# Optimization experiments

Measured on AMD Instinct MI355X. Metric: run time of the kernel, lower is better.

The kernel has to match this reference:

```python
import jax, jax.numpy as jnp
import numpy as np

B, NQ, NK = 16, 512, 1024
CQ, CV = 128, 128
H, D = 8, 64            # nb_heads, attention_size
SCALE = float(np.sqrt(D))


def setup_inputs() -> dict:
    key = jax.random.key(0)
    ks = jax.random.split(key, 10)
    s = 0.02
    return {
        "query": jax.random.normal(ks[0], (B, NQ, CQ), jnp.float32),
        "key": jax.random.normal(ks[1], (B, NK, CV), jnp.float32),
        "c_mask": jax.random.randint(ks[2], (B, NK), 0, 2).astype(jnp.float32),
        # torch Linear params, stored as [in, out] so y = x @ W + b
        "Wq": jax.random.normal(ks[3], (CQ, H * D), jnp.float32) * s,
        "bq": jnp.zeros((H * D,), jnp.float32),
        "Wk": jax.random.normal(ks[4], (CV, H * D), jnp.float32) * s,
        "bk": jnp.zeros((H * D,), jnp.float32),
        "Wv": jax.random.normal(ks[5], (CV, H * D), jnp.float32) * s,
        "bv": jnp.zeros((H * D,), jnp.float32),
    }


def reference(query, key, c_mask, Wq, bq, Wk, bk, Wv, bv):
    # projections -> [B, N, H, D]
    q = (query @ Wq + bq).reshape(B, NQ, H, D)
    k = (key @ Wk + bk).reshape(B, NK, H, D)
    v = (key @ Wv + bv).reshape(B, NK, H, D)
    # scaled scores [B, H, NQ, NK]
    scores = jnp.einsum('bqhd,bkhd->bhqk', q / SCALE, k)
    # additive mask: c_mask [B, NK] broadcasts over heads and queries
    scores = scores - 100000.0 * (1.0 - c_mask[:, None, None, :])
    attn = jax.nn.softmax(scores, axis=-1)
    # weighted values -> [B, NQ, H, D] -> concat heads
    c = jnp.einsum('bhqk,bkhd->bqhd', attn, v)
    return c.reshape(B, NQ, H * D)
```

## Files before the change

kernel.cpp:

```cpp
#include <hip/hip_runtime.h>
#include <hip/hip_bf16.h>

#define B_  16
#define NQ_ 512
#define NK_ 1024
#define CQ_ 128
#define H_  8
#define D_  64
#define HD_ 512

typedef __attribute__((ext_vector_type(8))) short short8;
typedef __attribute__((ext_vector_type(4))) float floatx4;

__device__ __forceinline__ short f2bf(float f) {
    union { float f; unsigned u; } x; x.f = f;
    unsigned r = (x.u + 0x7fffu + ((x.u >> 16) & 1u)) >> 16;
    return (short)r;
}
__device__ __forceinline__ int f2bf_pk(float a, float b) {
    __hip_bfloat162 h = __float22bfloat162_rn(make_float2(a, b));
    int r; __builtin_memcpy(&r, &h, 4); return r;
}
__device__ __forceinline__ short8 pack8(float4 a, float4 b) {
    union { int4 i; short8 s; } u;
    u.i = make_int4(f2bf_pk(a.x, a.y), f2bf_pk(a.z, a.w),
                    f2bf_pk(b.x, b.y), f2bf_pk(b.z, b.w));
    return u.s;
}
__device__ __forceinline__ int2 packi2(floatx4 a) {
    return make_int2(f2bf_pk(a[0], a[1]), f2bf_pk(a[2], a[3]));
}
__device__ __forceinline__ void async16(const short* g, short* l) {
    __builtin_amdgcn_global_load_lds(
        (const __attribute__((address_space(1))) void*)g,
        (__attribute__((address_space(3))) void*)l, 16, 0, 0);
}

__global__ __launch_bounds__(256) void prep_kernel(
    const float* __restrict__ W0, const float* __restrict__ W1,
    const float* __restrict__ W2, short* __restrict__ T0,
    short* __restrict__ T1, short* __restrict__ T2,
    const float* __restrict__ bq, float* __restrict__ bqs, float qscale)
{
    const int blk = blockIdx.x, t = threadIdx.x;
    if (blk == 48) {
        bqs[t]       = bq[t] * qscale;
        bqs[t + 256] = bq[t + 256] * qscale;
        return;
    }
    __shared__ short tsh[32 * 132];
    const int mat = blk >> 4, nb = blk & 15;
    const float* W = mat == 0 ? W0 : (mat == 1 ? W1 : W2);
    short* T = mat == 0 ? T0 : (mat == 1 ? T1 : T2);
    const float s = mat == 0 ? qscale : 1.0f;

    #pragma unroll
    for (int i = 0; i < 4; ++i) {
        const int idx = i * 256 + t;
        const int k = idx >> 3, c = (idx & 7) * 4;
        float4 v = *(const float4*)(W + (size_t)k * HD_ + nb * 32 + c);
        tsh[(c + 0) * 132 + k] = f2bf(v.x * s);
        tsh[(c + 1) * 132 + k] = f2bf(v.y * s);
        tsh[(c + 2) * 132 + k] = f2bf(v.z * s);
        tsh[(c + 3) * 132 + k] = f2bf(v.w * s);
    }
    __syncthreads();
    #pragma unroll
    for (int j = 0; j < 2; ++j) {
        const int idx = j * 256 + t;
        const int n = idx >> 4, seg = (idx & 15) * 8;
        *(short8*)(T + (size_t)(nb * 32 + n) * CQ_ + seg) =
            *(const short8*)&tsh[n * 132 + seg];
    }
}

__global__ __launch_bounds__(256, 2) void kvproj_kernel(
    const float* __restrict__ key_,
    const short* __restrict__ wkt, const short* __restrict__ wvt,
    const float* __restrict__ bk, const float* __restrict__ bv,
    short* __restrict__ ks, short* __restrict__ vt)
{
    __shared__ __align__(16) short csh[9216];

    int bx = blockIdx.x;
    const short* Wt; const float* bias; short* out; int transposed;
    if (bx < 128) { Wt = wkt; bias = bk; out = ks; transposed = 0; }
    else { bx -= 128; Wt = wvt; bias = bv; out = vt; transposed = 1; }

    const int tid  = threadIdx.x;
    const int w    = tid >> 6, lane = tid & 63;
    const int l15  = lane & 15, quad = lane >> 4;
    const int mbase = bx * 128;

    short8 afr[2][4];
    #pragma unroll
    for (int mt = 0; mt < 2; ++mt) {
        const float* xrow = key_ + (size_t)(mbase + w * 32 + mt * 16 + l15) * CQ_;
        #pragma unroll
        for (int kt = 0; kt < 4; ++kt)
            afr[mt][kt] = pack8(*(const float4*)(xrow + kt * 32 + quad * 8),
                                *(const float4*)(xrow + kt * 32 + quad * 8 + 4));
    }

    const int b  = mbase >> 10;
    const int r0 = mbase & 1023;

    #pragma unroll
    for (int hh = 0; hh < 4; ++hh) {
        const int h = blockIdx.y * 4 + hh;
        short8 bfr[4][4];
        #pragma unroll
        for (int nt = 0; nt < 4; ++nt) {
            const short8* wrow = (const short8*)(Wt + (size_t)(h * 64 + nt * 16 + l15) * CQ_);
            #pragma unroll
            for (int kt = 0; kt < 4; ++kt) bfr[nt][kt] = wrow[kt * 4 + quad];
        }
        floatx4 acc[2][4];
        #pragma unroll
        for (int mt = 0; mt < 2; ++mt)
            #pragma unroll
            for (int nt = 0; nt < 4; ++nt) {
                floatx4 a = {0.f, 0.f, 0.f, 0.f};
                #pragma unroll
                for (int kt = 0; kt < 4; ++kt)
                    a = __builtin_amdgcn_mfma_f32_16x16x32_bf16(afr[mt][kt], bfr[nt][kt], a, 0, 0, 0);
                acc[mt][nt] = a;
            }
        __syncthreads();
        #pragma unroll
        for (int mt = 0; mt < 2; ++mt)
            #pragma unroll
            for (int nt = 0; nt < 4; ++nt) {
                const float bvv = bias[h * 64 + nt * 16 + l15];
                #pragma unroll
                for (int i = 0; i < 4; ++i) {
                    const short s = f2bf(acc[mt][nt][i] + bvv);
                    const int m = w * 32 + mt * 16 + quad * 4 + i;
                    const int n = nt * 16 + l15;
                    if (!transposed) csh[m * 72 + n]  = s;
                    else             csh[n * 136 + m] = s;
                }
            }
        __syncthreads();

        const size_t bh = (size_t)(b * H_ + h);
        if (!transposed) {
            short* dst = out + (bh * NK_ + r0) * D_;
            #pragma unroll
            for (int it = 0; it < 4; ++it) {
                const int idx = it * 256 + tid;
                const int row = idx >> 3, c8 = (idx & 7) * 8;
                *(short8*)(dst + idx * 8) = *(const short8*)&csh[row * 72 + c8];
            }
        } else {
            short* dst = out + bh * D_ * NK_ + r0;
            #pragma unroll
            for (int it = 0; it < 4; ++it) {
                const int idx = it * 256 + tid;
                const int row = idx >> 4, c8 = (idx & 15) * 8;
                *(short8*)(dst + (size_t)row * NK_ + c8) = *(const short8*)&csh[row * 136 + c8];
            }
        }
    }
}

__global__ __launch_bounds__(256, 2) void attn_kernel(
    const float* __restrict__ query, const short* __restrict__ ks,
    const short* __restrict__ vt, const float* __restrict__ cmask,
    const short* __restrict__ wqt, const float* __restrict__ bqs,
    float* __restrict__ out)
{
    __shared__ __align__(16) short kbuf[2][2][64 * 64];
    __shared__ __align__(16) short vbuf[2][2][64 * 64];
    __shared__ __align__(16) short psh[128 * 64];

    const int tid = threadIdx.x;
    const int w = tid >> 6, lane = tid & 63;
    const int l15 = lane & 15, quad = lane >> 4;

    const int bx   = blockIdx.x;
    const int bh_i = bx & 127;
    const int qq   = bx >> 7;
    const int h    = bh_i & 7;
    const int b    = bh_i >> 3;

    const size_t bh = (size_t)bh_i;
    const short* kb_ = ks + bh * NK_ * D_;
    const short* vb  = vt + bh * D_ * NK_;
    const float* mk  = cmask + (size_t)b * NK_;

    short8 qa[2][2];
    {
        short8 waf[4][4];
        #pragma unroll
        for (int dt = 0; dt < 4; ++dt)
            #pragma unroll
            for (int kt = 0; kt < 4; ++kt)
                waf[dt][kt] = *(const short8*)(wqt + (size_t)(h * 64 + dt * 16 + l15) * CQ_ + kt * 32 + quad * 8);
        const int qr0 = qq * 128 + w * 32;
        #pragma unroll
        for (int g = 0; g < 2; ++g) {
            const float* qrow = query + ((size_t)b * NQ_ + qr0 + g * 16 + l15) * CQ_;
            short8 bqf[4];
            #pragma unroll
            for (int kt = 0; kt < 4; ++kt)
                bqf[kt] = pack8(*(const float4*)(qrow + kt * 32 + quad * 8),
                                *(const float4*)(qrow + kt * 32 + quad * 8 + 4));
            const int prow = w * 32 + g * 16 + l15;
            #pragma unroll
            for (int dt = 0; dt < 4; ++dt) {
                float4 bi = *(const float4*)(bqs + h * 64 + dt * 16 + quad * 4);
                floatx4 a = {bi.x, bi.y, bi.z, bi.w};
                #pragma unroll
                for (int kt = 0; kt < 4; ++kt)
                    a = __builtin_amdgcn_mfma_f32_16x16x32_bf16(waf[dt][kt], bqf[kt], a, 0, 0, 0);
                const int c16 = (dt * 2 + (quad >> 1)) ^ (prow & 7);
                *(int2*)&psh[prow * 64 + c16 * 8 + (quad & 1) * 4] = packi2(a);
            }
            qa[g][0] = *(const short8*)&psh[prow * 64 + ((quad    ) ^ (prow & 7)) * 8];
            qa[g][1] = *(const short8*)&psh[prow * 64 + ((4 + quad) ^ (prow & 7)) * 8];
        }
    }

    const int srow8 = lane >> 3, sc = lane & 7;
    auto stage = [&](int kb0, short (*kdst)[4096], short (*vdst)[4096]) {
        #pragma unroll
        for (int sub = 0; sub < 2; ++sub)
            #pragma unroll
            for (int j = 0; j < 2; ++j) {
                const int row = w * 16 + j * 8 + srow8;
                const int cs = sc ^ (row & 7);
                async16(kb_ + (size_t)(kb0 + sub * 64 + row) * D_ + cs * 8,
                        &kdst[sub][(w * 16 + j * 8) * 64]);
                async16(vb + (size_t)row * NK_ + kb0 + sub * 64 + cs * 8,
                        &vdst[sub][(w * 16 + j * 8) * 64]);
            }
    };

    float l_lane[2] = {0.f, 0.f};
    floatx4 o_acc[2][4];
    #pragma unroll
    for (int g = 0; g < 2; ++g)
        #pragma unroll
        for (int dt = 0; dt < 4; ++dt) o_acc[g][dt] = (floatx4){0.f, 0.f, 0.f, 0.f};

    stage(0, kbuf[0], vbuf[0]);
    __syncthreads();

    for (int ph = 0; ph < 8; ++ph) {
        const int cur = ph & 1;
        if (ph < 7) stage((ph + 1) * 128, kbuf[cur ^ 1], vbuf[cur ^ 1]);

        #pragma unroll
        for (int sub = 0; sub < 2; ++sub) {
            const short* kb  = kbuf[cur][sub];
            const short* vbl = vbuf[cur][sub];
            const int kbase = ph * 128 + sub * 64;

            short8 ka[4][2];
            #pragma unroll
            for (int nt = 0; nt < 4; ++nt) {
                const int row = nt * 16 + l15;
                ka[nt][0] = *(const short8*)&kb[row * 64 + ((quad    ) ^ (row & 7)) * 8];
                ka[nt][1] = *(const short8*)&kb[row * 64 + ((4 + quad) ^ (row & 7)) * 8];
            }
            short8 vf[2][4];
            #pragma unroll
            for (int dt = 0; dt < 4; ++dt) {
                const int row = dt * 16 + l15;
                vf[0][dt] = *(const short8*)&vbl[row * 64 + ((quad    ) ^ (row & 7)) * 8];
                vf[1][dt] = *(const short8*)&vbl[row * 64 + ((4 + quad) ^ (row & 7)) * 8];
            }
            float4 m4[4];
            #pragma unroll
            for (int nt = 0; nt < 4; ++nt)
                m4[nt] = *(const float4*)(mk + kbase + nt * 16 + quad * 4);

            #pragma unroll
            for (int g = 0; g < 2; ++g) {
                floatx4 st[4];
                #pragma unroll
                for (int nt = 0; nt < 4; ++nt) {
                    floatx4 a = {0.f, 0.f, 0.f, 0.f};
                    a = __builtin_amdgcn_mfma_f32_16x16x32_bf16(ka[nt][1], qa[g][1], a, 0, 0, 0);
                    a = __builtin_amdgcn_mfma_f32_16x16x32_bf16(ka[nt][0], qa[g][0], a, 0, 0, 0);
                    st[nt] = a;
                }
                const int prow = w * 32 + g * 16 + l15;
                float psum = 0.f;
                #pragma unroll
                for (int nt = 0; nt < 4; ++nt) {
                    float p0 = m4[nt].x * __builtin_amdgcn_exp2f(st[nt][0]);
                    float p1 = m4[nt].y * __builtin_amdgcn_exp2f(st[nt][1]);
                    float p2 = m4[nt].z * __builtin_amdgcn_exp2f(st[nt][2]);
                    float p3 = m4[nt].w * __builtin_amdgcn_exp2f(st[nt][3]);
                    psum += (p0 + p1) + (p2 + p3);
                    int2 pk = make_int2(f2bf_pk(p0, p1), f2bf_pk(p2, p3));
                    const int c16 = (2 * nt + (quad >> 1)) ^ (prow & 7);
                    *(int2*)&psh[prow * 64 + c16 * 8 + (quad & 1) * 4] = pk;
                }
                l_lane[g] += psum;
                #pragma unroll
                for (int kt = 0; kt < 2; ++kt) {
                    short8 pa = *(const short8*)&psh[prow * 64 + ((kt * 4 + quad) ^ (prow & 7)) * 8];
                    #pragma unroll
                    for (int dt = 0; dt < 4; ++dt)
                        o_acc[g][dt] = __builtin_amdgcn_mfma_f32_16x16x32_bf16(vf[kt][dt], pa, o_acc[g][dt], 0, 0, 0);
                }
            }
        }
        __syncthreads();
    }

    #pragma unroll
    for (int g = 0; g < 2; ++g) {
        float ls = l_lane[g];
        ls += __shfl_xor(ls, 16);
        ls += __shfl_xor(ls, 32);
        const float linv = 1.0f / ls;
        const int qr = qq * 128 + w * 32 + g * 16 + l15;
        float* orow = out + ((size_t)b * NQ_ + qr) * HD_ + h * D_;
        #pragma unroll
        for (int dt = 0; dt < 4; ++dt) {
            float4 v = make_float4(o_acc[g][dt][0] * linv, o_acc[g][dt][1] * linv,
                                   o_acc[g][dt][2] * linv, o_acc[g][dt][3] * linv);
            *(float4*)(orow + dt * 16 + quad * 4) = v;
        }
    }
}

extern "C" void kernel_launch(void* const* d_in, const int* in_sizes, int n_in,
                              void* d_out, int out_size, void* d_ws, size_t ws_size,
                              hipStream_t stream) {
    const float* query = (const float*)d_in[0];
    const float* key   = (const float*)d_in[1];
    const float* cmask = (const float*)d_in[2];
    const float* Wq    = (const float*)d_in[3];
    const float* bq    = (const float*)d_in[4];
    const float* Wk    = (const float*)d_in[5];
    const float* bk    = (const float*)d_in[6];
    const float* Wv    = (const float*)d_in[7];
    const float* bv    = (const float*)d_in[8];
    float* out = (float*)d_out;

    char* ws = (char*)d_ws;
    short* ks  = (short*)(ws);
    short* vt  = (short*)(ws + (size_t)(16u << 20));
    char*  w32 = ws + (size_t)(32u << 20);
    short* wqt = (short*)(w32);
    short* wkt = (short*)(w32 + 131072);
    short* wvt = (short*)(w32 + 131072 * 2);
    float* bqs = (float*)(w32 + 131072 * 3);

    const float qscale = 0.125f * 1.44269504f;
    prep_kernel<<<dim3(49), dim3(256), 0, stream>>>(
        Wq, Wk, Wv, wqt, wkt, wvt, bq, bqs, qscale);

    kvproj_kernel<<<dim3(256, 2), dim3(256), 0, stream>>>(
        key, wkt, wvt, bk, bv, ks, vt);

    attn_kernel<<<dim3(512), dim3(256), 0, stream>>>(
        query, ks, vt, cmask, wqt, bqs, out);
}
```

Measured before the change: 146.7 us.

## Compact unmasked keys per batch and skip masked keys in projection and attention

The prep kernel gains extra blocks that prefix-scan each batch's key mask. Each block writes a compacted list of unmasked key indices, a compacted mask, and a padded count rounded up to 128. The K/V projection gathers only unmasked key rows and exits early past that count, and attention loops over 64-key chunks only up to the padded count. This removes the projection, MFMA and exp work for masked keys, which is roughly half of them with this mask. The cost is an extra scan pass, gathered row loads, and a smaller pipeline stage per iteration.

```diff
diff --git a/kernel.cpp b/kernel.cpp
--- a/kernel.cpp
+++ b/kernel.cpp
@@ -40,7 +40,9 @@
     const float* __restrict__ W0, const float* __restrict__ W1,
     const float* __restrict__ W2, short* __restrict__ T0,
     short* __restrict__ T1, short* __restrict__ T2,
-    const float* __restrict__ bq, float* __restrict__ bqs, float qscale)
+    const float* __restrict__ bq, float* __restrict__ bqs, float qscale,
+    const float* __restrict__ cmask, int* __restrict__ idx,
+    float* __restrict__ cm2, int* __restrict__ npad)
 {
     const int blk = blockIdx.x, t = threadIdx.x;
     if (blk == 48) {
@@ -48,16 +50,46 @@
         bqs[t + 256] = bq[t + 256] * qscale;
         return;
     }
+    if (blk >= 49) {
+        __shared__ int wsum[4];
+        const int b = blk - 49;
+        const int w = t >> 6, lane = t & 63;
+        float4 m4 = *(const float4*)(cmask + b * NK_ + t * 4);
+        const int m0 = m4.x > 0.5f, m1 = m4.y > 0.5f, m2 = m4.z > 0.5f, m3 = m4.w > 0.5f;
+        const int s = m0 + m1 + m2 + m3;
+        int v = s;
+        #pragma unroll
+        for (int off = 1; off < 64; off <<= 1) {
+            int u = __shfl_up(v, off);
+            if (lane >= off) v += u;
+        }
+        if (lane == 63) wsum[w] = v;
+        __syncthreads();
+        int pre = 0;
+        #pragma unroll
+        for (int i = 0; i < 4; ++i) if (i < w) pre += wsum[i];
+        int pos = pre + v - s;
+        const int base = b * NK_;
+        if (m0) { idx[base + pos] = t * 4 + 0; cm2[base + pos] = 1.0f; ++pos; }
+        if (m1) { idx[base + pos] = t * 4 + 1; cm2[base + pos] = 1.0f; ++pos; }
+        if (m2) { idx[base + pos] = t * 4 + 2; cm2[base + pos] = 1.0f; ++pos; }
+        if (m3) { idx[base + pos] = t * 4 + 3; cm2[base + pos] = 1.0f; ++pos; }
+        const int total = wsum[0] + wsum[1] + wsum[2] + wsum[3];
+        for (int j = total + t; j < NK_; j += 256) {
+            idx[base + j] = 0; cm2[base + j] = 0.0f;
+        }
+        if (t == 0) npad[b] = (total + 127) & ~127;
+        return;
+    }
     __shared__ short tsh[32 * 132];
     const int mat = blk >> 4, nb = blk & 15;
     const float* W = mat == 0 ? W0 : (mat == 1 ? W1 : W2);
     short* T = mat == 0 ? T0 : (mat == 1 ? T1 : T2);
     const float s = mat == 0 ? qscale : 1.0f;
-
     #pragma unroll
     for (int i = 0; i < 4; ++i) {
-        const int idx = i * 256 + t;
-        const int k = idx >> 3, c = (idx & 7) * 4;
+        const int i2 = i * 256 + t;
+        const int k = i2 >> 3, c = (i2 & 7) * 4;
         float4 v = *(const float4*)(W + (size_t)k * HD_ + nb * 32 + c);
         tsh[(c + 0) * 132 + k] = f2bf(v.x * s);
         tsh[(c + 1) * 132 + k] = f2bf(v.y * s);
@@ -67,8 +99,8 @@
     __syncthreads();
     #pragma unroll
     for (int j = 0; j < 2; ++j) {
-        const int idx = j * 256 + t;
-        const int n = idx >> 4, seg = (idx & 15) * 8;
+        const int i2 = j * 256 + t;
+        const int n = i2 >> 4, seg = (i2 & 15) * 8;
         *(short8*)(T + (size_t)(nb * 32 + n) * CQ_ + seg) =
             *(const short8*)&tsh[n * 132 + seg];
     }
@@ -78,7 +110,8 @@
     const float* __restrict__ key_,
     const short* __restrict__ wkt, const short* __restrict__ wvt,
     const float* __restrict__ bk, const float* __restrict__ bv,
-    short* __restrict__ ks, short* __restrict__ vt)
+    short* __restrict__ ks, short* __restrict__ vt,
+    const int* __restrict__ idx, const int* __restrict__ npad)
 {
     __shared__ __align__(16) short csh[9216];
 
@@ -87,23 +120,26 @@
     if (bx < 128) { Wt = wkt; bias = bk; out = ks; transposed = 0; }
     else { bx -= 128; Wt = wvt; bias = bv; out = vt; transposed = 1; }
 
+    const int mbase = bx * 128;
+    const int b  = mbase >> 10;
+    const int r0 = mbase & 1023;
+    if (r0 >= npad[b]) return;
+
     const int tid  = threadIdx.x;
     const int w    = tid >> 6, lane = tid & 63;
     const int l15  = lane & 15, quad = lane >> 4;
-    const int mbase = bx * 128;
+    const int* ib = idx + b * NK_;
 
     short8 afr[2][4];
     #pragma unroll
     for (int mt = 0; mt < 2; ++mt) {
-        const float* xrow = key_ + (size_t)(mbase + w * 32 + mt * 16 + l15) * CQ_;
+        const int krow = ib[r0 + w * 32 + mt * 16 + l15];
+        const float* xrow = key_ + (size_t)(b * NK_ + krow) * CQ_;
         #pragma unroll
         for (int kt = 0; kt < 4; ++kt)
             afr[mt][kt] = pack8(*(const float4*)(xrow + kt * 32 + quad * 8),
                                 *(const float4*)(xrow + kt * 32 + quad * 8 + 4));
     }
-
-    const int b  = mbase >> 10;
-    const int r0 = mbase & 1023;
 
     #pragma unroll
     for (int hh = 0; hh < 4; ++hh) {
@@ -148,16 +184,16 @@
             short* dst = out + (bh * NK_ + r0) * D_;
             #pragma unroll
             for (int it = 0; it < 4; ++it) {
-                const int idx = it * 256 + tid;
-                const int row = idx >> 3, c8 = (idx & 7) * 8;
-                *(short8*)(dst + idx * 8) = *(const short8*)&csh[row * 72 + c8];
+                const int i2 = it * 256 + tid;
+                const int row = i2 >> 3, c8 = (i2 & 7) * 8;
+                *(short8*)(dst + i2 * 8) = *(const short8*)&csh[row * 72 + c8];
             }
         } else {
             short* dst = out + bh * D_ * NK_ + r0;
             #pragma unroll
             for (int it = 0; it < 4; ++it) {
-                const int idx = it * 256 + tid;
-                const int row = idx >> 4, c8 = (idx & 15) * 8;
+                const int i2 = it * 256 + tid;
+                const int row = i2 >> 4, c8 = (i2 & 15) * 8;
                 *(short8*)(dst + (size_t)row * NK_ + c8) = *(const short8*)&csh[row * 136 + c8];
             }
         }
@@ -166,12 +202,12 @@
 
 __global__ __launch_bounds__(256, 2) void attn_kernel(
     const float* __restrict__ query, const short* __restrict__ ks,
-    const short* __restrict__ vt, const float* __restrict__ cmask,
+    const short* __restrict__ vt, const float* __restrict__ cm2,
     const short* __restrict__ wqt, const float* __restrict__ bqs,
-    float* __restrict__ out)
+    const int* __restrict__ npad, float* __restrict__ out)
 {
-    __shared__ __align__(16) short kbuf[2][2][64 * 64];
-    __shared__ __align__(16) short vbuf[2][2][64 * 64];
+    __shared__ __align__(16) short kbuf[2][64 * 64];
+    __shared__ __align__(16) short vbuf[2][64 * 64];
     __shared__ __align__(16) short psh[128 * 64];
 
     const int tid = threadIdx.x;
@@ -187,7 +223,8 @@
     const size_t bh = (size_t)bh_i;
     const short* kb_ = ks + bh * NK_ * D_;
     const short* vb  = vt + bh * D_ * NK_;
-    const float* mk  = cmask + (size_t)b * NK_;
+    const float* mk  = cm2 + (size_t)b * NK_;
+    const int nc = npad[b] >> 6;
 
     short8 qa[2][2];
     {
@@ -223,18 +260,14 @@
     }
 
     const int srow8 = lane >> 3, sc = lane & 7;
-    auto stage = [&](int kb0, short (*kdst)[4096], short (*vdst)[4096]) {
-        #pragma unroll
-        for (int sub = 0; sub < 2; ++sub)
-            #pragma unroll
-            for (int j = 0; j < 2; ++j) {
-                const int row = w * 16 + j * 8 + srow8;
-                const int cs = sc ^ (row & 7);
-                async16(kb_ + (size_t)(kb0 + sub * 64 + row) * D_ + cs * 8,
-                        &kdst[sub][(w * 16 + j * 8) * 64]);
-                async16(vb + (size_t)row * NK_ + kb0 + sub * 64 + cs * 8,
-                        &vdst[sub][(w * 16 + j * 8) * 64]);
-            }
+    auto stage = [&](int kb0, short* kdst, short* vdst) {
+        #pragma unroll
+        for (int j = 0; j < 2; ++j) {
+            const int row = w * 16 + j * 8 + srow8;
+            const int cs = sc ^ (row & 7);
+            async16(kb_ + (size_t)(kb0 + row) * D_ + cs * 8, &kdst[(w * 16 + j * 8) * 64]);
+            async16(vb + (size_t)row * NK_ + kb0 + cs * 8, &vdst[(w * 16 + j * 8) * 64]);
+        }
     };
 
     float l_lane[2] = {0.f, 0.f};
@@ -247,66 +280,62 @@
     stage(0, kbuf[0], vbuf[0]);
     __syncthreads();
 
-    for (int ph = 0; ph < 8; ++ph) {
-        const int cur = ph & 1;
-        if (ph < 7) stage((ph + 1) * 128, kbuf[cur ^ 1], vbuf[cur ^ 1]);
-
-        #pragma unroll
-        for (int sub = 0; sub < 2; ++sub) {
-            const short* kb  = kbuf[cur][sub];
-            const short* vbl = vbuf[cur][sub];
-            const int kbase = ph * 128 + sub * 64;
-
-            short8 ka[4][2];
+    for (int t = 0; t < nc; ++t) {
+        const int cur = t & 1;
+        if (t + 1 < nc) stage((t + 1) * 64, kbuf[cur ^ 1], vbuf[cur ^ 1]);
+        const short* kb  = kbuf[cur];
+        const short* vbl = vbuf[cur];
+        const int kbase = t * 64;
+
+        short8 ka[4][2];
+        #pragma unroll
+        for (int nt = 0; nt < 4; ++nt) {
+            const int row = nt * 16 + l15;
+            ka[nt][0] = *(const short8*)&kb[row * 64 + ((quad    ) ^ (row & 7)) * 8];
+            ka[nt][1] = *(const short8*)&kb[row * 64 + ((4 + quad) ^ (row & 7)) * 8];
+        }
+        short8 vf[2][4];
+        #pragma unroll
+        for (int dt = 0; dt < 4; ++dt) {
+            const int row = dt * 16 + l15;
+            vf[0][dt] = *(const short8*)&vbl[row * 64 + ((quad    ) ^ (row & 7)) * 8];
+            vf[1][dt] = *(const short8*)&vbl[row * 64 + ((4 + quad) ^ (row & 7)) * 8];
+        }
+        float4 m4[4];
+        #pragma unroll
+        for (int nt = 0; nt < 4; ++nt)
+            m4[nt] = *(const float4*)(mk + kbase + nt * 16 + quad * 4);
+
+        #pragma unroll
+        for (int g = 0; g < 2; ++g) {
+            floatx4 st[4];
             #pragma unroll
             for (int nt = 0; nt < 4; ++nt) {
-                const int row = nt * 16 + l15;
-                ka[nt][0] = *(const short8*)&kb[row * 64 + ((quad    ) ^ (row & 7)) * 8];
-                ka[nt][1] = *(const short8*)&kb[row * 64 + ((4 + quad) ^ (row & 7)) * 8];
-            }
-            short8 vf[2][4];
-            #pragma unroll
-            for (int dt = 0; dt < 4; ++dt) {
-                const int row = dt * 16 + l15;
-                vf[0][dt] = *(const short8*)&vbl[row * 64 + ((quad    ) ^ (row & 7)) * 8];
-                vf[1][dt] = *(const short8*)&vbl[row * 64 + ((4 + quad) ^ (row & 7)) * 8];
-            }
-            float4 m4[4];
-            #pragma unroll
-            for (int nt = 0; nt < 4; ++nt)
-                m4[nt] = *(const float4*)(mk + kbase + nt * 16 + quad * 4);
-
-            #pragma unroll
-            for (int g = 0; g < 2; ++g) {
-                floatx4 st[4];
+                floatx4 a = {0.f, 0.f, 0.f, 0.f};
+                a = __builtin_amdgcn_mfma_f32_16x16x32_bf16(ka[nt][1], qa[g][1], a, 0, 0, 0);
+                a = __builtin_amdgcn_mfma_f32_16x16x32_bf16(ka[nt][0], qa[g][0], a, 0, 0, 0);
+                st[nt] = a;
+            }
+            const int prow = w * 32 + g * 16 + l15;
+            float psum = 0.f;
+            #pragma unroll
+            for (int nt = 0; nt < 4; ++nt) {
+                float p0 = m4[nt].x * __builtin_amdgcn_exp2f(st[nt][0]);
+                float p1 = m4[nt].y * __builtin_amdgcn_exp2f(st[nt][1]);
+                float p2 = m4[nt].z * __builtin_amdgcn_exp2f(st[nt][2]);
+                float p3 = m4[nt].w * __builtin_amdgcn_exp2f(st[nt][3]);
+                psum += (p0 + p1) + (p2 + p3);
+                int2 pk = make_int2(f2bf_pk(p0, p1), f2bf_pk(p2, p3));
+                const int c16 = (2 * nt + (quad >> 1)) ^ (prow & 7);
+                *(int2*)&psh[prow * 64 + c16 * 8 + (quad & 1) * 4] = pk;
+            }
+            l_lane[g] += psum;
+            #pragma unroll
+            for (int kt = 0; kt < 2; ++kt) {
+                short8 pa = *(const short8*)&psh[prow * 64 + ((kt * 4 + quad) ^ (prow & 7)) * 8];
                 #pragma unroll
-                for (int nt = 0; nt < 4; ++nt) {
-                    floatx4 a = {0.f, 0.f, 0.f, 0.f};
-                    a = __builtin_amdgcn_mfma_f32_16x16x32_bf16(ka[nt][1], qa[g][1], a, 0, 0, 0);
-                    a = __builtin_amdgcn_mfma_f32_16x16x32_bf16(ka[nt][0], qa[g][0], a, 0, 0, 0);
-                    st[nt] = a;
-                }
-                const int prow = w * 32 + g * 16 + l15;
-                float psum = 0.f;
-                #pragma unroll
-                for (int nt = 0; nt < 4; ++nt) {
-                    float p0 = m4[nt].x * __builtin_amdgcn_exp2f(st[nt][0]);
-                    float p1 = m4[nt].y * __builtin_amdgcn_exp2f(st[nt][1]);
-                    float p2 = m4[nt].z * __builtin_amdgcn_exp2f(st[nt][2]);
-                    float p3 = m4[nt].w * __builtin_amdgcn_exp2f(st[nt][3]);
-                    psum += (p0 + p1) + (p2 + p3);
-                    int2 pk = make_int2(f2bf_pk(p0, p1), f2bf_pk(p2, p3));
-                    const int c16 = (2 * nt + (quad >> 1)) ^ (prow & 7);
-                    *(int2*)&psh[prow * 64 + c16 * 8 + (quad & 1) * 4] = pk;
-                }
-                l_lane[g] += psum;
-                #pragma unroll
-                for (int kt = 0; kt < 2; ++kt) {
-                    short8 pa = *(const short8*)&psh[prow * 64 + ((kt * 4 + quad) ^ (prow & 7)) * 8];
-                    #pragma unroll
-                    for (int dt = 0; dt < 4; ++dt)
-                        o_acc[g][dt] = __builtin_amdgcn_mfma_f32_16x16x32_bf16(vf[kt][dt], pa, o_acc[g][dt], 0, 0, 0);
-                }
+                for (int dt = 0; dt < 4; ++dt)
+                    o_acc[g][dt] = __builtin_amdgcn_mfma_f32_16x16x32_bf16(vf[kt][dt], pa, o_acc[g][dt], 0, 0, 0);
             }
         }
         __syncthreads();
@@ -351,14 +380,17 @@
     short* wkt = (short*)(w32 + 131072);
     short* wvt = (short*)(w32 + 131072 * 2);
     float* bqs = (float*)(w32 + 131072 * 3);
+    int*   idx = (int*)(w32 + 131072 * 3 + 4096);
+    float* cm2 = (float*)(w32 + 131072 * 3 + 4096 + 65536);
+    int*  npad = (int*)(w32 + 131072 * 3 + 4096 + 131072);
 
     const float qscale = 0.125f * 1.44269504f;
-    prep_kernel<<<dim3(49), dim3(256), 0, stream>>>(
-        Wq, Wk, Wv, wqt, wkt, wvt, bq, bqs, qscale);
+    prep_kernel<<<dim3(65), dim3(256), 0, stream>>>(
+        Wq, Wk, Wv, wqt, wkt, wvt, bq, bqs, qscale, cmask, idx, cm2, npad);
 
     kvproj_kernel<<<dim3(256, 2), dim3(256), 0, stream>>>(
-        key, wkt, wvt, bk, bv, ks, vt);
+        key, wkt, wvt, bk, bv, ks, vt, idx, npad);
 
     attn_kernel<<<dim3(512), dim3(256), 0, stream>>>(
-        query, ks, vt, cmask, wqt, bqs, out);
-}
+        query, ks, vt, cm2, wqt, bqs, npad, out);
+}
```

New measurement: 135.6 us. -7.6%, faster.
